# Optimization experiments

Hardware: AMD Instinct MI355X
Metric: run time of the kernel (lower is better)

Reference implementation:

```python
import jax, jax.numpy as jnp
import numpy as np

N = 50000       # nodes
E = 1600000     # edges
G = 16          # graphs in batch
NUMCHIP = 16    # node features
NUMEDGE = 8     # edge features
H = 32          # hidden_channels
NEG = 0.2       # LeakyReLU slope (PyG GAT default)


def _wegat_conv(x, ea, src, dst, Wn, bn, We, be, att):
    """Edge-weighted GAT conv: returns (node_out [N,H], edge_out [E,NUMEDGE])."""
    xn = x @ Wn + bn                      # [N, H]
    ea2 = ea @ We + be                    # [E, NUMEDGE]
    xi = xn[dst]                          # [E, H] target features
    xj = xn[src]                          # [E, H] source features
    logits = jnp.concatenate([xi, xj, ea2], axis=-1) @ att   # [E]
    logits = jax.nn.leaky_relu(logits, NEG)
    # numerically stable softmax over incoming edges per destination node
    m = jax.ops.segment_max(logits, dst, num_segments=N)
    m = jnp.where(jnp.isfinite(m), m, 0.0)
    p = jnp.exp(logits - m[dst])
    s = jax.ops.segment_sum(p, dst, num_segments=N)
    alpha = p / (s[dst] + 1e-16)          # [E]
    out = jax.ops.segment_sum(xj * alpha[:, None], dst, num_segments=N)  # [N, H]
    return out, ea2


def setup_inputs() -> dict:
    key = jax.random.key(0)
    ks = jax.random.split(key, 24)

    def gl(k, shape):
        fan_in = shape[0] if len(shape) > 1 else shape[0]
        return jax.random.normal(k, shape, dtype=jnp.float32) * (1.0 / np.sqrt(fan_in))

    inp = {
        'x': jax.random.normal(ks[0], (N, NUMCHIP), dtype=jnp.float32),
        'edge_attr': jax.random.normal(ks[1], (E, NUMEDGE), dtype=jnp.float32),
        'edge_index': jax.random.randint(ks[2], (2, E), 0, N, dtype=jnp.int64),
        'batch': jnp.sort(jax.random.randint(ks[3], (N,), 0, G, dtype=jnp.int64)),
        # layer 1
        'Wn1': gl(ks[4], (NUMCHIP, H)), 'bn1': jnp.zeros((H,), jnp.float32),
        'We1': gl(ks[5], (NUMEDGE, NUMEDGE)), 'be1': jnp.zeros((NUMEDGE,), jnp.float32),
        'att1': gl(ks[6], (2 * H + NUMEDGE,)),
        # layer 2
        'Wn2': gl(ks[7], (H, H)), 'bn2': jnp.zeros((H,), jnp.float32),
        'We2': gl(ks[8], (NUMEDGE, NUMEDGE)), 'be2': jnp.zeros((NUMEDGE,), jnp.float32),
        'att2': gl(ks[9], (2 * H + NUMEDGE,)),
        # layer 3
        'Wn3': gl(ks[10], (H, H)), 'bn3': jnp.zeros((H,), jnp.float32),
        'We3': gl(ks[11], (NUMEDGE, NUMEDGE)), 'be3': jnp.zeros((NUMEDGE,), jnp.float32),
        'att3': gl(ks[12], (2 * H + NUMEDGE,)),
        # head
        'Wlin': gl(ks[13], (H, 1)), 'blin': jnp.zeros((1,), jnp.float32),
    }
    return inp


def reference(x, edge_attr, edge_index, batch,
              Wn1, bn1, We1, be1, att1,
              Wn2, bn2, We2, be2, att2,
              Wn3, bn3, We3, be3, att3,
              Wlin, blin):
    src, dst = edge_index[0], edge_index[1]
    x1, ea1 = _wegat_conv(x, edge_attr, src, dst, Wn1, bn1, We1, be1, att1)
    x1 = jax.nn.relu(x1)  # NOTE: original's edge_attr.relu() is a discarded no-op
    x2, ea2 = _wegat_conv(x1, ea1, src, dst, Wn2, bn2, We2, be2, att2)
    x2 = jax.nn.relu(x2)
    x3, _ = _wegat_conv(x2, ea2, src, dst, Wn3, bn3, We3, be3, att3)
    # global mean pool over graphs
    sums = jax.ops.segment_sum(x3, batch, num_segments=G)                   # [G, H]
    cnts = jax.ops.segment_sum(jnp.ones((N,), x3.dtype), batch, num_segments=G)
    pooled = sums / jnp.maximum(cnts, 1.0)[:, None]
    return pooled @ Wlin + blin  # [G, 1]
```

## Files before the change

### kernel.cpp

```cpp
#include <hip/hip_runtime.h>
#include <math.h>


__global__ __launch_bounds__(256) void hist_kernel(const int* __restrict__ dst, int* cnt, int E) {
    int e = blockIdx.x * blockDim.x + threadIdx.x;
    if (e < E) atomicAdd(&cnt[dst[e]], 1);
}

__global__ __launch_bounds__(1024) void scan_kernel(const int* __restrict__ cnt,
                                                    int* rowptr, int* cursor, int n) {
    __shared__ int sums[1024];
    int t = threadIdx.x;
    int CH = (n + 1023) >> 10;
    int s0 = t * CH;
    int s1 = min(n, s0 + CH);
    int local = 0;
    for (int i = s0; i < s1; i++) local += cnt[i];
    sums[t] = local;
    __syncthreads();
    for (int off = 1; off < 1024; off <<= 1) {
        int v = (t >= off) ? sums[t - off] : 0;
        __syncthreads();
        sums[t] += v;
        __syncthreads();
    }
    int run = (t == 0) ? 0 : sums[t - 1];
    for (int i = s0; i < s1; i++) {
        rowptr[i] = run;
        cursor[i] = run;
        run += cnt[i];
    }
    if (t == 1023) rowptr[n] = sums[1023];
}

__global__ __launch_bounds__(256) void scatter_kernel(const int* __restrict__ src,
                                                      const int* __restrict__ dst,
                                                      int* cursor, int2* __restrict__ pack, int E) {
    int e = blockIdx.x * blockDim.x + threadIdx.x;
    if (e >= E) return;
    int d = dst[e];
    int pos = atomicAdd(&cursor[d], 1);
    pack[pos] = make_int2(src[e], e);
}

template <int IN>
__global__ __launch_bounds__(256) void node_linear(const float* __restrict__ xin,
                                                   const float* __restrict__ Wn,
                                                   const float* __restrict__ bn,
                                                   const float* __restrict__ att,
                                                   float* __restrict__ xn,
                                                   float* __restrict__ ai,
                                                   float* __restrict__ aj, int n) {
    int t = blockIdx.x * blockDim.x + threadIdx.x;
    int node = t >> 5;
    int h = t & 31;
    if (node >= n) return;
    float acc = bn[h];
#pragma unroll
    for (int k = 0; k < IN; k++) {
        acc = fmaf(xin[node * IN + k], Wn[k * 32 + h], acc);
    }
    xn[node * 32 + h] = acc;
    float pi = acc * att[h];
    float pj = acc * att[32 + h];
#pragma unroll
    for (int off = 16; off > 0; off >>= 1) {
        pi += __shfl_xor(pi, off);
        pj += __shfl_xor(pj, off);
    }
    if (h == 0) {
        ai[node] = pi;
        aj[node] = pj;
    }
}

__global__ __launch_bounds__(256) void edge_chain(
    const float* __restrict__ ein,
    const float* __restrict__ We1, const float* __restrict__ be1, const float* __restrict__ a1,
    const float* __restrict__ We2, const float* __restrict__ be2, const float* __restrict__ a2,
    const float* __restrict__ We3, const float* __restrict__ be3, const float* __restrict__ a3,
    float* __restrict__ ae1, float* __restrict__ ae2, float* __restrict__ ae3, int E) {
    int e = blockIdx.x * blockDim.x + threadIdx.x;
    if (e >= E) return;
    const float4* p = (const float4*)(ein + (size_t)e * 8);
    float4 x0 = p[0], x1 = p[1];
    float v[8] = {x0.x, x0.y, x0.z, x0.w, x1.x, x1.y, x1.z, x1.w};
    float t[8], u[8];
    float d1 = 0.f, d2 = 0.f, d3 = 0.f;
#pragma unroll
    for (int j = 0; j < 8; j++) {
        float a = be1[j];
#pragma unroll
        for (int k = 0; k < 8; k++) a = fmaf(v[k], We1[k * 8 + j], a);
        t[j] = a;
        d1 = fmaf(a, a1[j], d1);
    }
#pragma unroll
    for (int j = 0; j < 8; j++) {
        float a = be2[j];
#pragma unroll
        for (int k = 0; k < 8; k++) a = fmaf(t[k], We2[k * 8 + j], a);
        u[j] = a;
        d2 = fmaf(a, a2[j], d2);
    }
#pragma unroll
    for (int j = 0; j < 8; j++) {
        float a = be3[j];
#pragma unroll
        for (int k = 0; k < 8; k++) a = fmaf(u[k], We3[k * 8 + j], a);
        d3 = fmaf(a, a3[j], d3);
    }
    ae1[e] = d1;
    ae2[e] = d2;
    ae3[e] = d3;
}

__global__ __launch_bounds__(256) void gat_aggregate(const float* __restrict__ xn,
                                                     const float* __restrict__ ai,
                                                     const float* __restrict__ aj,
                                                     const float* __restrict__ ae,
                                                     const int* __restrict__ rowptr,
                                                     const int2* __restrict__ pack,
                                                     float* __restrict__ xout,
                                                     int n, int relu_out) {
    int wave = (blockIdx.x * blockDim.x + threadIdx.x) >> 6;
    int lane = threadIdx.x & 63;
    if (wave >= n) return;
    int node = wave;
    int row = rowptr[node];
    int deg = rowptr[node + 1] - row;
    int h = lane & 31;
    if (deg == 0) {
        if (lane < 32) xout[node * 32 + h] = 0.f;
        return;
    }
    float a_i = ai[node];
    const int2* pk = pack + row;

    float mx = -INFINITY;
    for (int k = lane; k < deg; k += 64) {
        int2 q = pk[k];
        float lg = a_i + aj[q.x] + ae[q.y];
        lg = (lg >= 0.f) ? lg : 0.2f * lg;
        mx = fmaxf(mx, lg);
    }
#pragma unroll
    for (int off = 32; off > 0; off >>= 1) mx = fmaxf(mx, __shfl_xor(mx, off));

    float acc = 0.f, psum = 0.f;
    int half = lane >> 5;
    for (int base = 0; base < deg; base += 64) {
        int k = base + lane;
        float p = 0.f;
        int s = 0;
        if (k < deg) {
            int2 q = pk[k];
            s = q.x;
            float lg = a_i + aj[s] + ae[q.y];
            lg = (lg >= 0.f) ? lg : 0.2f * lg;
            p = expf(lg - mx);
        }
        psum += p;
        int csize = min(64, deg - base);
        for (int j = half; j < csize; j += 2) {
            float pj = __shfl(p, j);
            int sj = __shfl(s, j);
            acc = fmaf(pj, xn[sj * 32 + h], acc);
        }
    }
#pragma unroll
    for (int off = 32; off > 0; off >>= 1) psum += __shfl_xor(psum, off);
    acc += __shfl_xor(acc, 32);

    float o = acc / (psum + 1e-16f);
    if (relu_out) o = fmaxf(o, 0.f);
    if (lane < 32) xout[node * 32 + h] = o;
}

__global__ __launch_bounds__(256) void pool_kernel(const float* __restrict__ x3,
                                                   const int* __restrict__ batch,
                                                   float* pool, int n) {
    int h = threadIdx.x & 31;
    int rowl = threadIdx.x >> 5;
    int per = (n + gridDim.x - 1) / gridDim.x;
    int n0 = blockIdx.x * per;
    int n1 = min(n, n0 + per);
    float acc = 0.f;
    int curg = -1;
    for (int i = n0 + rowl; i < n1; i += 8) {
        int g = batch[i];
        if (g != curg) {
            if (curg >= 0) atomicAdd(&pool[curg * 32 + h], acc);
            acc = 0.f;
            curg = g;
        }
        acc += x3[i * 32 + h];
    }
    if (curg >= 0) atomicAdd(&pool[curg * 32 + h], acc);
}

__global__ __launch_bounds__(64) void head_kernel(const float* __restrict__ pool,
                                                  const int* __restrict__ batch,
                                                  const float* __restrict__ Wlin,
                                                  const float* __restrict__ blin,
                                                  float* out, int n, int G) {
    int g = threadIdx.x;
    if (g >= G) return;
    float s = 0.f;
#pragma unroll
    for (int k = 0; k < 32; k++) s = fmaf(pool[g * 32 + k], Wlin[k], s);
    int lo = 0, hi = n;
    while (lo < hi) {
        int m = (lo + hi) >> 1;
        if (batch[m] < g) lo = m + 1; else hi = m;
    }
    int start = lo;
    lo = 0; hi = n;
    while (lo < hi) {
        int m = (lo + hi) >> 1;
        if (batch[m] < g + 1) lo = m + 1; else hi = m;
    }
    float c = fmaxf((float)(lo - start), 1.f);
    out[g] = s / c + blin[0];
}

extern "C" void kernel_launch(void* const* d_in, const int* in_sizes, int n_in,
                              void* d_out, int out_size, void* d_ws, size_t ws_size,
                              hipStream_t stream) {
    const float* x    = (const float*)d_in[0];
    const float* ea0  = (const float*)d_in[1];
    const int* ei     = (const int*)d_in[2];
    const int* batch  = (const int*)d_in[3];
    const float* Wn[3] = {(const float*)d_in[4], (const float*)d_in[9],  (const float*)d_in[14]};
    const float* bn[3] = {(const float*)d_in[5], (const float*)d_in[10], (const float*)d_in[15]};
    const float* We[3] = {(const float*)d_in[6], (const float*)d_in[11], (const float*)d_in[16]};
    const float* be[3] = {(const float*)d_in[7], (const float*)d_in[12], (const float*)d_in[17]};
    const float* att[3]= {(const float*)d_in[8], (const float*)d_in[13], (const float*)d_in[18]};
    const float* Wlin = (const float*)d_in[19];
    const float* blin = (const float*)d_in[20];
    float* out = (float*)d_out;

    const int N = in_sizes[0] / 16;
    const int E = in_sizes[1] / 8;
    const int G = out_size;
    (void)n_in; (void)ws_size;

    const int* srcp = ei;
    const int* dstp = ei + E;

    char* base = (char*)d_ws;
    size_t off = 0;
    auto carve = [&](size_t bytes) -> void* {
        void* p = base + off;
        off = (off + bytes + 255) & ~(size_t)255;
        return p;
    };
    float* xnA   = (float*)carve((size_t)N * 32 * 4);
    float* xnB   = (float*)carve((size_t)N * 32 * 4);
    float* ai    = (float*)carve((size_t)N * 4);
    float* aj    = (float*)carve((size_t)N * 4);
    float* ae1   = (float*)carve((size_t)E * 4);
    float* ae2   = (float*)carve((size_t)E * 4);
    float* ae3   = (float*)carve((size_t)E * 4);
    int* cnt     = (int*)carve((size_t)N * 4);
    int* rowptr  = (int*)carve((size_t)(N + 1) * 4);
    int* cursor  = (int*)carve((size_t)N * 4);
    int2* pack   = (int2*)carve((size_t)E * 8);
    float* pool  = (float*)carve((size_t)G * 32 * 4);

    int ebks = (E + 255) / 256;
    int nhbks = (N * 32 + 255) / 256;
    int aggbks = (N + 3) / 4;

    hipMemsetAsync(cnt, 0, (size_t)N * 4, stream);
    hipMemsetAsync(pool, 0, (size_t)G * 32 * 4, stream);
    hist_kernel<<<ebks, 256, 0, stream>>>(dstp, cnt, E);
    scan_kernel<<<1, 1024, 0, stream>>>(cnt, rowptr, cursor, N);
    scatter_kernel<<<ebks, 256, 0, stream>>>(srcp, dstp, cursor, pack, E);

    edge_chain<<<ebks, 256, 0, stream>>>(ea0,
                                         We[0], be[0], att[0] + 64,
                                         We[1], be[1], att[1] + 64,
                                         We[2], be[2], att[2] + 64,
                                         ae1, ae2, ae3, E);

    node_linear<16><<<nhbks, 256, 0, stream>>>(x, Wn[0], bn[0], att[0], xnA, ai, aj, N);
    gat_aggregate<<<aggbks, 256, 0, stream>>>(xnA, ai, aj, ae1, rowptr, pack, xnB, N, 1);

    node_linear<32><<<nhbks, 256, 0, stream>>>(xnB, Wn[1], bn[1], att[1], xnA, ai, aj, N);
    gat_aggregate<<<aggbks, 256, 0, stream>>>(xnA, ai, aj, ae2, rowptr, pack, xnB, N, 1);

    node_linear<32><<<nhbks, 256, 0, stream>>>(xnB, Wn[2], bn[2], att[2], xnA, ai, aj, N);
    gat_aggregate<<<aggbks, 256, 0, stream>>>(xnA, ai, aj, ae3, rowptr, pack, xnB, N, 0);

    pool_kernel<<<128, 256, 0, stream>>>(xnB, batch, pool, N);
    head_kernel<<<1, 64, 0, stream>>>(pool, batch, Wlin, blin, out, N, G);
}
```

Baseline: 741.4 us.

## Make CSR build and aggregation deterministic with bucketed sort and sequential reductions

```diff
diff --git a/kernel.cpp b/kernel.cpp
--- a/kernel.cpp
+++ b/kernel.cpp
@@ -1,6 +1,10 @@
 #include <hip/hip_runtime.h>
 #include <math.h>
 
+
+#define P1_TILE 4096
+#define P2_CAP  7808
+#define MAXD    512
 
 __global__ __launch_bounds__(256) void hist_kernel(const int* __restrict__ dst, int* cnt, int E) {
     int e = blockIdx.x * blockDim.x + threadIdx.x;
@@ -33,14 +37,112 @@
     if (t == 1023) rowptr[n] = sums[1023];
 }
 
-__global__ __launch_bounds__(256) void scatter_kernel(const int* __restrict__ src,
+__global__ __launch_bounds__(512) void init_bcur(const int* __restrict__ rowptr,
+                                                 int* bcur, int n, int nb) {
+    int b = blockIdx.x * blockDim.x + threadIdx.x;
+    if (b < nb) bcur[b] = rowptr[min(n, b << 7)];
+}
+
+__global__ __launch_bounds__(512) void bucket_scatter(const int* __restrict__ src,
                                                       const int* __restrict__ dst,
-                                                      int* cursor, int2* __restrict__ pack, int E) {
-    int e = blockIdx.x * blockDim.x + threadIdx.x;
-    if (e >= E) return;
-    int d = dst[e];
-    int pos = atomicAdd(&cursor[d], 1);
-    pack[pos] = make_int2(src[e], e);
+                                                      int* bcur, int2* __restrict__ bsort,
+                                                      int E) {
+    __shared__ int2 stage[P1_TILE];
+    __shared__ int dest[P1_TILE];
+    __shared__ int lcnt[512], sc[512], lbase[512], lgbase[512], lpos[512];
+    int t = threadIdx.x;
+    int tile0 = blockIdx.x * P1_TILE;
+    int cnt_here = min(P1_TILE, E - tile0);
+    lcnt[t] = 0;
+    __syncthreads();
+#pragma unroll
+    for (int r = 0; r < P1_TILE / 512; r++) {
+        int i = t + (r << 9);
+        if (i < cnt_here) atomicAdd(&lcnt[dst[tile0 + i] >> 7], 1);
+    }
+    __syncthreads();
+    sc[t] = lcnt[t];
+    __syncthreads();
+    for (int off = 1; off < 512; off <<= 1) {
+        int v = (t >= off) ? sc[t - off] : 0;
+        __syncthreads();
+        sc[t] += v;
+        __syncthreads();
+    }
+    lbase[t] = sc[t] - lcnt[t];
+    lpos[t] = lbase[t];
+    if (lcnt[t] > 0) lgbase[t] = atomicAdd(&bcur[t], lcnt[t]) - lbase[t];
+    __syncthreads();
+#pragma unroll
+    for (int r = 0; r < P1_TILE / 512; r++) {
+        int i = t + (r << 9);
+        if (i < cnt_here) {
+            int e = tile0 + i;
+            int d = dst[e];
+            int b = d >> 7;
+            int loc = atomicAdd(&lpos[b], 1);
+            stage[loc] = make_int2(src[e], (e << 7) | (d & 127));
+            dest[loc] = lgbase[b] + loc;
+        }
+    }
+    __syncthreads();
+    for (int i = t; i < cnt_here; i += 512) bsort[dest[i]] = stage[i];
+}
+
+__global__ __launch_bounds__(1024) void bucket_sort(const int2* __restrict__ bsort,
+                                                    const int* __restrict__ rowptr,
+                                                    int* cursor,
+                                                    int2* __restrict__ pack, int n) {
+    __shared__ int2 lpack[P2_CAP];
+    __shared__ int lcur[129];
+    int bk = blockIdx.x;
+    int node0 = bk << 7;
+    int nodes = min(128, n - node0);
+    int r0 = rowptr[node0];
+    int r1 = rowptr[min(n, node0 + 128)];
+    int cnt = r1 - r0;
+    int t = threadIdx.x;
+    if (t < nodes) lcur[t] = rowptr[node0 + t] - r0;
+    __syncthreads();
+    if (cnt <= P2_CAP) {
+        for (int i = t; i < cnt; i += 1024) {
+            int2 q = bsort[r0 + i];
+            int dl = q.y & 127;
+            int pos = atomicAdd(&lcur[dl], 1);
+            lpack[pos] = make_int2(q.x, ((unsigned)q.y) >> 7);
+        }
+        __syncthreads();
+        for (int i = t; i < cnt; i += 1024) pack[r0 + i] = lpack[i];
+    } else {
+        for (int i = t; i < cnt; i += 1024) {
+            int2 q = bsort[r0 + i];
+            int dl = q.y & 127;
+            int pos = atomicAdd(&cursor[node0 + dl], 1);
+            pack[pos] = make_int2(q.x, ((unsigned)q.y) >> 7);
+        }
+    }
+}
+
+__global__ __launch_bounds__(256) void sort_pass(const int* __restrict__ rowptr,
+                                                 int2* __restrict__ pack, int n) {
+    __shared__ int2 buf[4][MAXD];
+    int wl = threadIdx.x >> 6, lane = threadIdx.x & 63;
+    int node = (blockIdx.x << 2) + wl;
+    int row = 0, deg = 0;
+    if (node < n) { row = rowptr[node]; deg = rowptr[node + 1] - row; }
+    bool doit = (deg > 1 && deg <= MAXD);
+    if (doit) {
+        for (int k = lane; k < deg; k += 64) buf[wl][k] = pack[row + k];
+    }
+    __syncthreads();
+    if (doit) {
+        for (int k = lane; k < deg; k += 64) {
+            int2 mine = buf[wl][k];
+            int rank = 0;
+            for (int m = 0; m < deg; m++) rank += (buf[wl][m].y < mine.y);
+            pack[row + rank] = mine;
+        }
+    }
 }
 
 template <int IN>
@@ -85,21 +187,21 @@
     const float4* p = (const float4*)(ein + (size_t)e * 8);
     float4 x0 = p[0], x1 = p[1];
     float v[8] = {x0.x, x0.y, x0.z, x0.w, x1.x, x1.y, x1.z, x1.w};
-    float t[8], u[8];
+    float tt[8], u[8];
     float d1 = 0.f, d2 = 0.f, d3 = 0.f;
 #pragma unroll
     for (int j = 0; j < 8; j++) {
         float a = be1[j];
 #pragma unroll
         for (int k = 0; k < 8; k++) a = fmaf(v[k], We1[k * 8 + j], a);
-        t[j] = a;
+        tt[j] = a;
         d1 = fmaf(a, a1[j], d1);
     }
 #pragma unroll
     for (int j = 0; j < 8; j++) {
         float a = be2[j];
 #pragma unroll
-        for (int k = 0; k < 8; k++) a = fmaf(t[k], We2[k * 8 + j], a);
+        for (int k = 0; k < 8; k++) a = fmaf(tt[k], We2[k * 8 + j], a);
         u[j] = a;
         d2 = fmaf(a, a2[j], d2);
     }
@@ -123,105 +225,93 @@
                                                      const int2* __restrict__ pack,
                                                      float* __restrict__ xout,
                                                      int n, int relu_out) {
-    int wave = (blockIdx.x * blockDim.x + threadIdx.x) >> 6;
-    int lane = threadIdx.x & 63;
-    if (wave >= n) return;
-    int node = wave;
+    int t = threadIdx.x;
+    int node = blockIdx.x * 8 + (t >> 5);
+    int h = t & 31;
+    if (node >= n) return;
     int row = rowptr[node];
     int deg = rowptr[node + 1] - row;
-    int h = lane & 31;
-    if (deg == 0) {
-        if (lane < 32) xout[node * 32 + h] = 0.f;
-        return;
-    }
+    if (deg == 0) { xout[node * 32 + h] = 0.f; return; }
     float a_i = ai[node];
     const int2* pk = pack + row;
 
     float mx = -INFINITY;
-    for (int k = lane; k < deg; k += 64) {
+    for (int k = h; k < deg; k += 32) {
         int2 q = pk[k];
         float lg = a_i + aj[q.x] + ae[q.y];
         lg = (lg >= 0.f) ? lg : 0.2f * lg;
         mx = fmaxf(mx, lg);
     }
 #pragma unroll
-    for (int off = 32; off > 0; off >>= 1) mx = fmaxf(mx, __shfl_xor(mx, off));
-
-    float acc = 0.f, psum = 0.f;
-    int half = lane >> 5;
-    for (int base = 0; base < deg; base += 64) {
-        int k = base + lane;
-        float p = 0.f;
-        int s = 0;
-        if (k < deg) {
-            int2 q = pk[k];
-            s = q.x;
-            float lg = a_i + aj[s] + ae[q.y];
-            lg = (lg >= 0.f) ? lg : 0.2f * lg;
-            p = expf(lg - mx);
-        }
-        psum += p;
-        int csize = min(64, deg - base);
-        for (int j = half; j < csize; j += 2) {
-            float pj = __shfl(p, j);
-            int sj = __shfl(s, j);
-            acc = fmaf(pj, xn[sj * 32 + h], acc);
-        }
-    }
-#pragma unroll
-    for (int off = 32; off > 0; off >>= 1) psum += __shfl_xor(psum, off);
-    acc += __shfl_xor(acc, 32);
-
-    float o = acc / (psum + 1e-16f);
-    if (relu_out) o = fmaxf(o, 0.f);
-    if (lane < 32) xout[node * 32 + h] = o;
-}
-
-__global__ __launch_bounds__(256) void pool_kernel(const float* __restrict__ x3,
-                                                   const int* __restrict__ batch,
-                                                   float* pool, int n) {
-    int h = threadIdx.x & 31;
-    int rowl = threadIdx.x >> 5;
-    int per = (n + gridDim.x - 1) / gridDim.x;
-    int n0 = blockIdx.x * per;
-    int n1 = min(n, n0 + per);
+    for (int off = 16; off > 0; off >>= 1) mx = fmaxf(mx, __shfl_xor(mx, off));
+
+    float psum = 0.f;
+    for (int k = 0; k < deg; k++) {
+        int2 q = pk[k];
+        float lg = a_i + aj[q.x] + ae[q.y];
+        lg = (lg >= 0.f) ? lg : 0.2f * lg;
+        float p = expf(lg - mx);
+        psum = __fadd_rn(psum, p);
+    }
+    float denom = __fadd_rn(psum, 1e-16f);
+
     float acc = 0.f;
-    int curg = -1;
-    for (int i = n0 + rowl; i < n1; i += 8) {
-        int g = batch[i];
-        if (g != curg) {
-            if (curg >= 0) atomicAdd(&pool[curg * 32 + h], acc);
-            acc = 0.f;
-            curg = g;
-        }
-        acc += x3[i * 32 + h];
-    }
-    if (curg >= 0) atomicAdd(&pool[curg * 32 + h], acc);
-}
-
-__global__ __launch_bounds__(64) void head_kernel(const float* __restrict__ pool,
-                                                  const int* __restrict__ batch,
-                                                  const float* __restrict__ Wlin,
-                                                  const float* __restrict__ blin,
-                                                  float* out, int n, int G) {
+    for (int k = 0; k < deg; k++) {
+        int2 q = pk[k];
+        float lg = a_i + aj[q.x] + ae[q.y];
+        lg = (lg >= 0.f) ? lg : 0.2f * lg;
+        float p = expf(lg - mx);
+        float alpha = __fdiv_rn(p, denom);
+        float xv = xn[q.x * 32 + h];
+        acc = __fadd_rn(acc, __fmul_rn(xv, alpha));
+    }
+    if (relu_out) acc = fmaxf(acc, 0.f);
+    xout[node * 32 + h] = acc;
+}
+
+__global__ __launch_bounds__(64) void pool_seq(const float* __restrict__ x3,
+                                               const int* __restrict__ batch,
+                                               float* __restrict__ pooled, int n) {
+    if (threadIdx.x != 0) return;
+    int g = blockIdx.x >> 5;
+    int h = blockIdx.x & 31;
+    int lo = 0, hi = n;
+    while (lo < hi) { int m = (lo + hi) >> 1; if (batch[m] < g) lo = m + 1; else hi = m; }
+    int start = lo;
+    lo = 0; hi = n;
+    while (lo < hi) { int m = (lo + hi) >> 1; if (batch[m] < g + 1) lo = m + 1; else hi = m; }
+    int end = lo;
+    float acc = 0.f;
+    int i = start;
+    for (; i + 8 <= end; i += 8) {
+        float v0 = x3[(i + 0) * 32 + h];
+        float v1 = x3[(i + 1) * 32 + h];
+        float v2 = x3[(i + 2) * 32 + h];
+        float v3 = x3[(i + 3) * 32 + h];
+        float v4 = x3[(i + 4) * 32 + h];
+        float v5 = x3[(i + 5) * 32 + h];
+        float v6 = x3[(i + 6) * 32 + h];
+        float v7 = x3[(i + 7) * 32 + h];
+        acc = __fadd_rn(acc, v0); acc = __fadd_rn(acc, v1);
+        acc = __fadd_rn(acc, v2); acc = __fadd_rn(acc, v3);
+        acc = __fadd_rn(acc, v4); acc = __fadd_rn(acc, v5);
+        acc = __fadd_rn(acc, v6); acc = __fadd_rn(acc, v7);
+    }
+    for (; i < end; i++) acc = __fadd_rn(acc, x3[i * 32 + h]);
+    float c = fmaxf((float)(end - start), 1.f);
+    pooled[g * 32 + h] = __fdiv_rn(acc, c);
+}
+
+__global__ __launch_bounds__(64) void head_np(const float* __restrict__ pooled,
+                                              const float* __restrict__ Wlin,
+                                              const float* __restrict__ blin,
+                                              float* __restrict__ out, int G) {
     int g = threadIdx.x;
     if (g >= G) return;
-    float s = 0.f;
-#pragma unroll
-    for (int k = 0; k < 32; k++) s = fmaf(pool[g * 32 + k], Wlin[k], s);
-    int lo = 0, hi = n;
-    while (lo < hi) {
-        int m = (lo + hi) >> 1;
-        if (batch[m] < g) lo = m + 1; else hi = m;
-    }
-    int start = lo;
-    lo = 0; hi = n;
-    while (lo < hi) {
-        int m = (lo + hi) >> 1;
-        if (batch[m] < g + 1) lo = m + 1; else hi = m;
-    }
-    float c = fmaxf((float)(lo - start), 1.f);
-    out[g] = s / c + blin[0];
+    float acc = 0.f;
+    for (int k = 0; k < 32; k++)
+        acc = __fadd_rn(acc, __fmul_rn(pooled[g * 32 + k], Wlin[k]));
+    out[g] = __fadd_rn(acc, blin[0]);
 }
 
 extern "C" void kernel_launch(void* const* d_in, const int* in_sizes, int n_in,
@@ -243,6 +333,7 @@
     const int N = in_sizes[0] / 16;
     const int E = in_sizes[1] / 8;
     const int G = out_size;
+    const int nb = (N + 127) >> 7;
     (void)n_in; (void)ws_size;
 
     const int* srcp = ei;
@@ -255,28 +346,34 @@
         off = (off + bytes + 255) & ~(size_t)255;
         return p;
     };
-    float* xnA   = (float*)carve((size_t)N * 32 * 4);
-    float* xnB   = (float*)carve((size_t)N * 32 * 4);
-    float* ai    = (float*)carve((size_t)N * 4);
-    float* aj    = (float*)carve((size_t)N * 4);
-    float* ae1   = (float*)carve((size_t)E * 4);
-    float* ae2   = (float*)carve((size_t)E * 4);
-    float* ae3   = (float*)carve((size_t)E * 4);
-    int* cnt     = (int*)carve((size_t)N * 4);
-    int* rowptr  = (int*)carve((size_t)(N + 1) * 4);
-    int* cursor  = (int*)carve((size_t)N * 4);
-    int2* pack   = (int2*)carve((size_t)E * 8);
-    float* pool  = (float*)carve((size_t)G * 32 * 4);
+    float* xnA    = (float*)carve((size_t)N * 32 * 4);
+    float* xnB    = (float*)carve((size_t)N * 32 * 4);
+    float* ai     = (float*)carve((size_t)N * 4);
+    float* aj     = (float*)carve((size_t)N * 4);
+    float* ae1    = (float*)carve((size_t)E * 4);
+    float* ae2    = (float*)carve((size_t)E * 4);
+    float* ae3    = (float*)carve((size_t)E * 4);
+    int* cnt      = (int*)carve((size_t)N * 4);
+    int* rowptr   = (int*)carve((size_t)(N + 1) * 4);
+    int* cursor   = (int*)carve((size_t)N * 4);
+    int* bcur     = (int*)carve((size_t)nb * 4);
+    int2* pack    = (int2*)carve((size_t)E * 8);
+    float* pooled = (float*)carve((size_t)G * 32 * 4);
+    int2* bsort = (((size_t)E * 4 % 256) == 0) ? (int2*)ae1
+                                               : (int2*)carve((size_t)E * 8);
 
     int ebks = (E + 255) / 256;
     int nhbks = (N * 32 + 255) / 256;
-    int aggbks = (N + 3) / 4;
+    int aggbks = (N + 7) / 8;
+    int srtbks = (N + 3) / 4;
 
     hipMemsetAsync(cnt, 0, (size_t)N * 4, stream);
-    hipMemsetAsync(pool, 0, (size_t)G * 32 * 4, stream);
     hist_kernel<<<ebks, 256, 0, stream>>>(dstp, cnt, E);
     scan_kernel<<<1, 1024, 0, stream>>>(cnt, rowptr, cursor, N);
-    scatter_kernel<<<ebks, 256, 0, stream>>>(srcp, dstp, cursor, pack, E);
+    init_bcur<<<(nb + 511) / 512, 512, 0, stream>>>(rowptr, bcur, N, nb);
+    bucket_scatter<<<(E + P1_TILE - 1) / P1_TILE, 512, 0, stream>>>(srcp, dstp, bcur, bsort, E);
+    bucket_sort<<<nb, 1024, 0, stream>>>(bsort, rowptr, cursor, pack, N);
+    sort_pass<<<srtbks, 256, 0, stream>>>(rowptr, pack, N);
 
     edge_chain<<<ebks, 256, 0, stream>>>(ea0,
                                          We[0], be[0], att[0] + 64,
@@ -293,6 +390,6 @@
     node_linear<32><<<nhbks, 256, 0, stream>>>(xnB, Wn[2], bn[2], att[2], xnA, ai, aj, N);
     gat_aggregate<<<aggbks, 256, 0, stream>>>(xnA, ai, aj, ae3, rowptr, pack, xnB, N, 0);
 
-    pool_kernel<<<128, 256, 0, stream>>>(xnB, batch, pool, N);
-    head_kernel<<<1, 64, 0, stream>>>(pool, batch, Wlin, blin, out, N, G);
-}
+    pool_seq<<<G * 32, 64, 0, stream>>>(xnB, batch, pooled, N);
+    head_np<<<1, 64, 0, stream>>>(pooled, Wlin, blin, out, G);
+}
```

Result: slower. 1.250 ms (+68.6%).
